# Kernel optimization log

Hardware: AMD Instinct MI355X
Metric: run time of the kernel (lower is better)

The kernel has to match this reference:

```python
import jax, jax.numpy as jnp
import numpy as np

VOCAB, EMBED, HIDDEN = 32000, 512, 1024
BATCH, SEQ = 32, 48
PAD = 0


def setup_inputs() -> dict:
    key = jax.random.key(0)
    ks = jax.random.split(key, 10)
    s = 0.02
    emb = jax.random.normal(ks[0], (VOCAB, EMBED), jnp.float32) * s
    emb = emb.at[PAD].set(0.0)  # padding_idx row zeroed
    return {
        "inputs": jax.random.randint(ks[1], (BATCH, SEQ), 0, VOCAB),
        "hidden": jax.random.normal(ks[2], (BATCH, HIDDEN), jnp.float32),
        "cell": jax.random.normal(ks[3], (BATCH, HIDDEN), jnp.float32),
        "emb": emb,
        "W_ih": jax.random.normal(ks[4], (4 * HIDDEN, EMBED), jnp.float32) * s,
        "W_hh": jax.random.normal(ks[5], (4 * HIDDEN, HIDDEN), jnp.float32) * s,
        "b_ih": jnp.zeros((4 * HIDDEN,), jnp.float32),
        "b_hh": jnp.zeros((4 * HIDDEN,), jnp.float32),
        "fc_W": jax.random.normal(ks[6], (VOCAB, HIDDEN), jnp.float32) * s,
        "fc_b": jnp.zeros((VOCAB,), jnp.float32),
        "generate_len": 50,
    }


def reference(inputs, hidden, cell, emb, W_ih, W_hh, b_ih, b_hh, fc_W, fc_b, generate_len):
    # Training-path forward (dropout treated as identity for determinism).
    x = emb[inputs]                      # [B, S, E]
    xs = jnp.transpose(x, (1, 0, 2))     # [S, B, E] time-major

    def step(carry, x_t):
        h, c = carry
        gates = x_t @ W_ih.T + b_ih + h @ W_hh.T + b_hh  # [B, 4H]
        i, f, g, o = jnp.split(gates, 4, axis=-1)
        c_new = jax.nn.sigmoid(f) * c + jax.nn.sigmoid(i) * jnp.tanh(g)
        h_new = jax.nn.sigmoid(o) * jnp.tanh(c_new)
        logits = h_new @ fc_W.T + fc_b                   # [B, V]
        return (h_new, c_new), logits

    _, out = jax.lax.scan(step, (hidden, cell), xs)      # [S, B, V]
    return jnp.transpose(out, (1, 0, 2))                 # [B, S, V]
```

## Files before the change

### kernel.cpp

```cpp
#include <hip/hip_runtime.h>
#include <stdint.h>


typedef unsigned short u16;
typedef __attribute__((ext_vector_type(8))) short bf16x8;
typedef __attribute__((ext_vector_type(4))) float floatx4;
struct alignas(8) us4 { u16 x, y, z, w; };

#define BATCH 32
#define SEQ   48
#define EMBED 512
#define HID   1024
#define VOCAB 32000
#define MROWS (SEQ * BATCH)

__device__ __forceinline__ u16 f2bf(float f) {
  unsigned u = __float_as_uint(f);
  u += 0x7FFF + ((u >> 16) & 1);
  return (u16)(u >> 16);
}

__device__ __forceinline__ floatx4 mfma16(bf16x8 a, bf16x8 b, floatx4 c) {
  return __builtin_amdgcn_mfma_f32_16x16x32_bf16(a, b, c, 0, 0, 0);
}

typedef __attribute__((address_space(1))) unsigned int as1_uint;
typedef __attribute__((address_space(3))) unsigned int as3_uint;
__device__ __forceinline__ void gl_lds16(const void* g, void* l) {
  __builtin_amdgcn_global_load_lds((as1_uint*)g, (as3_uint*)l, 16, 0, 0);
}

__device__ __forceinline__ float sigmoidf_(float x) {
  return 1.0f / (1.0f + __expf(-x));
}

__global__ void cast_kernel(const float* __restrict__ in, u16* __restrict__ out, int n4) {
  int i = blockIdx.x * blockDim.x + threadIdx.x;
  if (i < n4) {
    float4 v = *(const float4*)(in + (size_t)i * 4);
    us4 o;
    o.x = f2bf(v.x); o.y = f2bf(v.y); o.z = f2bf(v.z); o.w = f2bf(v.w);
    *(us4*)(out + (size_t)i * 4) = o;
  }
}

__global__ void gather_kernel(const int* __restrict__ idx, const float* __restrict__ emb,
                              u16* __restrict__ X) {
  int bid = blockIdx.x;
  int s = bid >> 5, b = bid & 31;
  int t = idx[b * SEQ + s];
  const float* src = emb + (size_t)t * EMBED;
  u16* dst = X + (size_t)bid * EMBED;
  int e = threadIdx.x * 4;
  float4 v = *(const float4*)(src + e);
  us4 o;
  o.x = f2bf(v.x); o.y = f2bf(v.y); o.z = f2bf(v.z); o.w = f2bf(v.w);
  *(us4*)(dst + e) = o;
}

__global__ __launch_bounds__(256) void gemm_bt_kernel(
    const u16* __restrict__ A, const u16* __restrict__ B,
    const float* __restrict__ bias0, const float* __restrict__ bias1,
    float* __restrict__ C, int M, int N, int K, int out_mode) {
  __shared__ u16 As[128 * 64];
  __shared__ u16 Bs[128 * 64];

  const int tid = threadIdx.x;
  const int wave = tid >> 6, lane = tid & 63;
  const int l3 = lane >> 3, l7 = lane & 7;
  const int q = lane >> 4, rf = lane & 15;
  const int tn = blockIdx.x, tm = blockIdx.y;
  const int gm0 = tm * 128, gn0 = tn * 128;
  const int wm = (wave & 1) * 64, wn = (wave >> 1) * 64;

  floatx4 acc[4][4];
#pragma unroll
  for (int i = 0; i < 4; ++i)
#pragma unroll
    for (int j = 0; j < 4; ++j) acc[i][j] = (floatx4){0.f, 0.f, 0.f, 0.f};

  for (int k0 = 0; k0 < K; k0 += 64) {
#pragma unroll
    for (int i = 0; i < 4; ++i) {
      int e = wave * 4 + i;
      int r = e * 8 + l3;
      int qd = l7 ^ (r & 7);
      gl_lds16(A + (size_t)(gm0 + r) * K + k0 + qd * 8, (void*)(As + e * 512));
      gl_lds16(B + (size_t)(gn0 + r) * K + k0 + qd * 8, (void*)(Bs + e * 512));
    }
    __syncthreads();

#pragma unroll
    for (int kk = 0; kk < 64; kk += 32) {
      int jc = (kk >> 3) + q;
      bf16x8 af[4], bf[4];
#pragma unroll
      for (int mi = 0; mi < 4; ++mi) {
        int r = wm + mi * 16 + rf;
        af[mi] = *(const bf16x8*)(As + r * 64 + (jc ^ (r & 7)) * 8);
      }
#pragma unroll
      for (int ni = 0; ni < 4; ++ni) {
        int r = wn + ni * 16 + rf;
        bf[ni] = *(const bf16x8*)(Bs + r * 64 + (jc ^ (r & 7)) * 8);
      }
#pragma unroll
      for (int mi = 0; mi < 4; ++mi)
#pragma unroll
        for (int ni = 0; ni < 4; ++ni)
          acc[mi][ni] = mfma16(af[mi], bf[ni], acc[mi][ni]);
    }
    __syncthreads();
  }

#pragma unroll
  for (int ni = 0; ni < 4; ++ni) {
    int n = gn0 + wn + ni * 16 + rf;
    float bv = bias0[n];
    if (bias1) bv += bias1[n];
#pragma unroll
    for (int mi = 0; mi < 4; ++mi) {
#pragma unroll
      for (int r = 0; r < 4; ++r) {
        int m = gm0 + wm + mi * 16 + q * 4 + r;
        float val = acc[mi][ni][r] + bv;
        if (out_mode == 0) {
          C[(size_t)m * N + n] = val;
        } else {
          int b = m & 31, s = m >> 5;
          C[((size_t)b * SEQ + s) * N + n] = val;
        }
      }
    }
  }
}

__global__ __launch_bounds__(256) void lstm_step_kernel(
    const u16* __restrict__ h_prev,
    const u16* __restrict__ Whh,
    const float* __restrict__ xg,
    const float* __restrict__ c_in,
    float* __restrict__ c_out,
    u16* __restrict__ h_out) {
  const int u0 = blockIdx.x * 4;
  const int tid = threadIdx.x;
  const int wave = tid >> 6, lane = tid & 63;
  const int q = lane >> 4, rf = lane & 15;
  const int gate = rf >> 2, du = rf & 3;
  const int brow = gate * HID + u0 + du;

  floatx4 acc0 = {0.f, 0.f, 0.f, 0.f}, acc1 = {0.f, 0.f, 0.f, 0.f};
  const u16* wp = Whh + (size_t)brow * HID + wave * 256 + q * 8;
  const u16* a0p = h_prev + (size_t)rf * HID + wave * 256 + q * 8;
  const u16* a1p = a0p + 16 * HID;
#pragma unroll
  for (int ks = 0; ks < 256; ks += 32) {
    bf16x8 bv = *(const bf16x8*)(wp + ks);
    bf16x8 a0 = *(const bf16x8*)(a0p + ks);
    bf16x8 a1 = *(const bf16x8*)(a1p + ks);
    acc0 = mfma16(a0, bv, acc0);
    acc1 = mfma16(a1, bv, acc1);
  }

  __shared__ float red[4][32][16];
#pragma unroll
  for (int r = 0; r < 4; ++r) {
    red[wave][q * 4 + r][rf] = acc0[r];
    red[wave][16 + q * 4 + r][rf] = acc1[r];
  }
  __syncthreads();

  if (tid < 128) {
    int b = tid >> 2, d = tid & 3;
    int u = u0 + d;
    float g4[4];
#pragma unroll
    for (int gt = 0; gt < 4; ++gt) {
      int n = gt * 4 + d;
      float v = red[0][b][n] + red[1][b][n] + red[2][b][n] + red[3][b][n];
      v += xg[b * 4096 + gt * HID + u];
      g4[gt] = v;
    }
    float i_ = sigmoidf_(g4[0]);
    float f_ = sigmoidf_(g4[1]);
    float gg = tanhf(g4[2]);
    float o_ = sigmoidf_(g4[3]);
    float c = f_ * c_in[b * HID + u] + i_ * gg;
    float h = o_ * tanhf(c);
    c_out[b * HID + u] = c;
    h_out[b * HID + u] = f2bf(h);
  }
}

extern "C" void kernel_launch(void* const* d_in, const int* in_sizes, int n_in,
                              void* d_out, int out_size, void* d_ws, size_t ws_size,
                              hipStream_t stream) {
  const int*   inputs = (const int*)d_in[0];
  const float* hidden = (const float*)d_in[1];
  const float* cell   = (const float*)d_in[2];
  const float* emb    = (const float*)d_in[3];
  const float* W_ih   = (const float*)d_in[4];
  const float* W_hh   = (const float*)d_in[5];
  const float* b_ih   = (const float*)d_in[6];
  const float* b_hh   = (const float*)d_in[7];
  const float* fc_W   = (const float*)d_in[8];
  const float* fc_b   = (const float*)d_in[9];
  float* out = (float*)d_out;

  char* ws = (char*)d_ws;
  u16*   Xbf  = (u16*)(ws);
  u16*   Wihb = (u16*)(ws + 1572864);
  u16*   Whhb = (u16*)(ws + 1572864 + 4194304);
  u16*   fcWb = (u16*)(ws + 14155776);
  float* Xg   = (float*)(ws + 14155776 + 65536000);
  u16*   Hall = (u16*)(ws + 104857600);
  float* c_ws = (float*)(ws + 104857600 + 3211264);

  cast_kernel<<<(4096 * 512 / 4 + 255) / 256, 256, 0, stream>>>(W_ih, Wihb, 4096 * 512 / 4);
  cast_kernel<<<(4096 * 1024 / 4 + 255) / 256, 256, 0, stream>>>(W_hh, Whhb, 4096 * 1024 / 4);
  cast_kernel<<<(VOCAB * 1024 / 4 + 255) / 256, 256, 0, stream>>>(fc_W, fcWb, VOCAB * 1024 / 4);
  cast_kernel<<<(BATCH * HID / 4 + 255) / 256, 256, 0, stream>>>(hidden, Hall, BATCH * HID / 4);

  gather_kernel<<<MROWS, 128, 0, stream>>>(inputs, emb, Xbf);

  gemm_bt_kernel<<<dim3(4096 / 128, MROWS / 128), 256, 0, stream>>>(
      Xbf, Wihb, b_ih, b_hh, Xg, MROWS, 4096, EMBED, 0);

  for (int s = 0; s < SEQ; ++s) {
    lstm_step_kernel<<<256, 256, 0, stream>>>(
        Hall + (size_t)s * BATCH * HID, Whhb, Xg + (size_t)s * BATCH * 4096,
        (s == 0) ? cell : c_ws, c_ws, Hall + (size_t)(s + 1) * BATCH * HID);
  }

  gemm_bt_kernel<<<dim3(VOCAB / 128, MROWS / 128), 256, 0, stream>>>(
      Hall + (size_t)BATCH * HID, fcWb, fc_b, (const float*)nullptr, out,
      MROWS, VOCAB, HID, 1);
}
```

Baseline: 819.2 us.

## Fuse LSTM timesteps into one persistent kernel with grid barrier

Replaces the 48 per-step LSTM kernel launches with a single persistent kernel of 64 workgroups that loops over time, keeps the cell state in registers, stages h in LDS, and synchronises steps through an atomic grid barrier. W_hh is pre-packed into an MFMA-friendly per-workgroup layout. The GEMM also gets a block-index swizzle that remaps tiles across XCDs for better L2 locality. The change removes launch overhead and redundant c traffic, but uses only 64 CUs per step and relies on all workgroups being co-resident for the spin barrier.

```diff
diff --git a/kernel.cpp b/kernel.cpp
--- a/kernel.cpp
+++ b/kernel.cpp
@@ -13,6 +13,7 @@
 #define HID   1024
 #define VOCAB 32000
 #define MROWS (SEQ * BATCH)
+#define NWG   64
 
 __device__ __forceinline__ u16 f2bf(float f) {
   unsigned u = __float_as_uint(f);
@@ -42,6 +43,20 @@
     o.x = f2bf(v.x); o.y = f2bf(v.y); o.z = f2bf(v.z); o.w = f2bf(v.w);
     *(us4*)(out + (size_t)i * 4) = o;
   }
+}
+
+__global__ void pack_whh_kernel(const float* __restrict__ Whh, u16* __restrict__ out) {
+  int t = blockIdx.x * blockDim.x + threadIdx.x;
+  int rf = t & 15;
+  int kc = (t >> 4) & 127;
+  int gw = t >> 11;
+  int g = gw >> 2, w = gw & 3;
+  const float* src = Whh + ((size_t)(w * 1024 + g * 16 + rf)) * HID + kc * 8;
+  float4 v0 = *(const float4*)(src);
+  float4 v1 = *(const float4*)(src + 4);
+  u16 o[8] = {f2bf(v0.x), f2bf(v0.y), f2bf(v0.z), f2bf(v0.w),
+              f2bf(v1.x), f2bf(v1.y), f2bf(v1.z), f2bf(v1.w)};
+  *(bf16x8*)(out + (size_t)t * 8) = *(bf16x8*)o;
 }
 
 __global__ void gather_kernel(const int* __restrict__ idx, const float* __restrict__ emb,
@@ -69,7 +84,21 @@
   const int wave = tid >> 6, lane = tid & 63;
   const int l3 = lane >> 3, l7 = lane & 7;
   const int q = lane >> 4, rf = lane & 15;
-  const int tn = blockIdx.x, tm = blockIdx.y;
+
+  int tm, tn;
+  {
+    int l = blockIdx.y * gridDim.x + blockIdx.x;
+    int total = gridDim.x * gridDim.y;
+    if ((total & 7) == 0) {
+      int per = total >> 3;
+      int seq = (l & 7) * per + (l >> 3);
+      int mt = gridDim.y;
+      tm = seq % mt;
+      tn = seq / mt;
+    } else {
+      tn = blockIdx.x; tm = blockIdx.y;
+    }
+  }
   const int gm0 = tm * 128, gn0 = tn * 128;
   const int wm = (wave & 1) * 64, wn = (wave >> 1) * 64;
 
@@ -135,60 +164,85 @@
   }
 }
 
-__global__ __launch_bounds__(256) void lstm_step_kernel(
-    const u16* __restrict__ h_prev,
-    const u16* __restrict__ Whh,
+__global__ __launch_bounds__(256) void lstm_persist_kernel(
+    const u16* __restrict__ Whhp,
     const float* __restrict__ xg,
-    const float* __restrict__ c_in,
-    float* __restrict__ c_out,
-    u16* __restrict__ h_out) {
-  const int u0 = blockIdx.x * 4;
+    const float* __restrict__ cell,
+    u16* __restrict__ Hall,
+    unsigned int* bar) {
+  __shared__ u16 hs[32 * HID];
+  __shared__ float gsh[4][32][16];
+
+  const int g = blockIdx.x;
   const int tid = threadIdx.x;
-  const int wave = tid >> 6, lane = tid & 63;
+  const int w = tid >> 6, lane = tid & 63;
   const int q = lane >> 4, rf = lane & 15;
-  const int gate = rf >> 2, du = rf & 3;
-  const int brow = gate * HID + u0 + du;
-
-  floatx4 acc0 = {0.f, 0.f, 0.f, 0.f}, acc1 = {0.f, 0.f, 0.f, 0.f};
-  const u16* wp = Whh + (size_t)brow * HID + wave * 256 + q * 8;
-  const u16* a0p = h_prev + (size_t)rf * HID + wave * 256 + q * 8;
-  const u16* a1p = a0p + 16 * HID;
-#pragma unroll
-  for (int ks = 0; ks < 256; ks += 32) {
-    bf16x8 bv = *(const bf16x8*)(wp + ks);
-    bf16x8 a0 = *(const bf16x8*)(a0p + ks);
-    bf16x8 a1 = *(const bf16x8*)(a1p + ks);
-    acc0 = mfma16(a0, bv, acc0);
-    acc1 = mfma16(a1, bv, acc1);
-  }
-
-  __shared__ float red[4][32][16];
-#pragma unroll
-  for (int r = 0; r < 4; ++r) {
-    red[wave][q * 4 + r][rf] = acc0[r];
-    red[wave][16 + q * 4 + r][rf] = acc1[r];
-  }
-  __syncthreads();
-
-  if (tid < 128) {
-    int b = tid >> 2, d = tid & 3;
-    int u = u0 + d;
-    float g4[4];
-#pragma unroll
-    for (int gt = 0; gt < 4; ++gt) {
-      int n = gt * 4 + d;
-      float v = red[0][b][n] + red[1][b][n] + red[2][b][n] + red[3][b][n];
-      v += xg[b * 4096 + gt * HID + u];
-      g4[gt] = v;
-    }
-    float i_ = sigmoidf_(g4[0]);
-    float f_ = sigmoidf_(g4[1]);
-    float gg = tanhf(g4[2]);
-    float o_ = sigmoidf_(g4[3]);
-    float c = f_ * c_in[b * HID + u] + i_ * gg;
-    float h = o_ * tanhf(c);
-    c_out[b * HID + u] = c;
-    h_out[b * HID + u] = f2bf(h);
+
+  const int b0 = tid >> 4, ul = tid & 15;
+  const int b1 = b0 + 16;
+  float c0 = cell[(size_t)b0 * HID + g * 16 + ul];
+  float c1 = cell[(size_t)b1 * HID + g * 16 + ul];
+
+  const u16* wbase = Whhp + (size_t)(g * 4 + w) * (128 * 128);
+  const float* xgl = xg + w * 1024 + g * 16 + rf;
+
+  for (int s = 0; s < SEQ; ++s) {
+    const u16* hsrc = Hall + (size_t)s * (32 * HID);
+#pragma unroll
+    for (int i = 0; i < 16; ++i) {
+      int ci = i * 256 + tid;
+      int row = ci >> 7, cj = ci & 127;
+      *(bf16x8*)(hs + (size_t)(row * 128 + (cj ^ (row & 7))) * 8) =
+          *(const bf16x8*)(hsrc + (size_t)ci * 8);
+    }
+    __syncthreads();
+
+    floatx4 acc0 = {0.f, 0.f, 0.f, 0.f}, acc1 = {0.f, 0.f, 0.f, 0.f};
+#pragma unroll 8
+    for (int it = 0; it < 32; ++it) {
+      int kc = it * 4 + q;
+      bf16x8 bfr = *(const bf16x8*)(wbase + (size_t)kc * 128 + rf * 8);
+      bf16x8 a0 = *(const bf16x8*)(hs + (size_t)(rf * 128 + (kc ^ (rf & 7))) * 8);
+      bf16x8 a1 = *(const bf16x8*)(hs + (size_t)((16 + rf) * 128 + (kc ^ (rf & 7))) * 8);
+      acc0 = mfma16(a0, bfr, acc0);
+      acc1 = mfma16(a1, bfr, acc1);
+    }
+
+    const float* xgs = xgl + (size_t)s * (32 * 4096);
+#pragma unroll
+    for (int r = 0; r < 4; ++r) {
+      gsh[w][q * 4 + r][rf]      = acc0[r] + xgs[(size_t)(q * 4 + r) * 4096];
+      gsh[w][16 + q * 4 + r][rf] = acc1[r] + xgs[(size_t)(16 + q * 4 + r) * 4096];
+    }
+    __syncthreads();
+
+    u16* hdst = Hall + (size_t)(s + 1) * (32 * HID) + g * 16;
+    {
+      float i_ = sigmoidf_(gsh[0][b0][ul]);
+      float f_ = sigmoidf_(gsh[1][b0][ul]);
+      float gg = tanhf(gsh[2][b0][ul]);
+      float o_ = sigmoidf_(gsh[3][b0][ul]);
+      c0 = f_ * c0 + i_ * gg;
+      hdst[(size_t)b0 * HID + ul] = f2bf(o_ * tanhf(c0));
+    }
+    {
+      float i_ = sigmoidf_(gsh[0][b1][ul]);
+      float f_ = sigmoidf_(gsh[1][b1][ul]);
+      float gg = tanhf(gsh[2][b1][ul]);
+      float o_ = sigmoidf_(gsh[3][b1][ul]);
+      c1 = f_ * c1 + i_ * gg;
+      hdst[(size_t)b1 * HID + ul] = f2bf(o_ * tanhf(c1));
+    }
+
+    __threadfence();
+    __syncthreads();
+    if (tid == 0) {
+      __hip_atomic_fetch_add(bar, 1u, __ATOMIC_RELEASE, __HIP_MEMORY_SCOPE_AGENT);
+      unsigned tgt = (unsigned)(s + 1) * NWG;
+      while (__hip_atomic_load(bar, __ATOMIC_ACQUIRE, __HIP_MEMORY_SCOPE_AGENT) < tgt)
+        __builtin_amdgcn_s_sleep(2);
+    }
+    __syncthreads();
   }
 }
 
@@ -210,14 +264,16 @@
   char* ws = (char*)d_ws;
   u16*   Xbf  = (u16*)(ws);
   u16*   Wihb = (u16*)(ws + 1572864);
-  u16*   Whhb = (u16*)(ws + 1572864 + 4194304);
+  u16*   Whhp = (u16*)(ws + 5767168);
   u16*   fcWb = (u16*)(ws + 14155776);
-  float* Xg   = (float*)(ws + 14155776 + 65536000);
+  float* Xg   = (float*)(ws + 79691776);
   u16*   Hall = (u16*)(ws + 104857600);
-  float* c_ws = (float*)(ws + 104857600 + 3211264);
+  unsigned int* bar = (unsigned int*)(ws + 108068864);
+
+  hipMemsetAsync((void*)bar, 0, sizeof(unsigned int), stream);
 
   cast_kernel<<<(4096 * 512 / 4 + 255) / 256, 256, 0, stream>>>(W_ih, Wihb, 4096 * 512 / 4);
-  cast_kernel<<<(4096 * 1024 / 4 + 255) / 256, 256, 0, stream>>>(W_hh, Whhb, 4096 * 1024 / 4);
+  pack_whh_kernel<<<(4096 * 1024 / 8) / 256, 256, 0, stream>>>(W_hh, Whhp);
   cast_kernel<<<(VOCAB * 1024 / 4 + 255) / 256, 256, 0, stream>>>(fc_W, fcWb, VOCAB * 1024 / 4);
   cast_kernel<<<(BATCH * HID / 4 + 255) / 256, 256, 0, stream>>>(hidden, Hall, BATCH * HID / 4);
 
@@ -226,11 +282,7 @@
   gemm_bt_kernel<<<dim3(4096 / 128, MROWS / 128), 256, 0, stream>>>(
       Xbf, Wihb, b_ih, b_hh, Xg, MROWS, 4096, EMBED, 0);
 
-  for (int s = 0; s < SEQ; ++s) {
-    lstm_step_kernel<<<256, 256, 0, stream>>>(
-        Hall + (size_t)s * BATCH * HID, Whhb, Xg + (size_t)s * BATCH * 4096,
-        (s == 0) ? cell : c_ws, c_ws, Hall + (size_t)(s + 1) * BATCH * HID);
-  }
+  lstm_persist_kernel<<<NWG, 256, 0, stream>>>(Whhp, Xg, cell, Hall, bar);
 
   gemm_bt_kernel<<<dim3(VOCAB / 128, MROWS / 128), 256, 0, stream>>>(
       Hall + (size_t)BATCH * HID, fcWb, fc_b, (const float*)nullptr, out,
```

After: 1.064 ms. 1.3x slower.
